# Kernel tuning notes

Measured on AMD Instinct MI355X. Metric: run time of the kernel, lower is better.

Reference implementation:

```python
import jax, jax.numpy as jnp
from jax import lax
import numpy as np


def _normalize(x):
    # F.normalize(dim=-1), eps=1e-12
    return x / jnp.clip(jnp.linalg.norm(x, axis=-1, keepdims=True), 1e-12, None)


def _masked_log_softmax(logits, mask):
    # softmax restricted to active columns (emulates gathering active objects)
    return jax.nn.log_softmax(jnp.where(mask, logits, -1e9), axis=-1)


def _aabb_iou(gc, gs, pc, ps):
    # gc,gs: (B,L,3) gt center/size; pc,ps: (B,P,3) pred center/size -> iou (B,L,P)
    # create_box_batch builds axis-aligned corner boxes, so box3d_overlap == AABB IoU
    gmin = (gc - gs * 0.5)[:, :, None, :]
    gmax = (gc + gs * 0.5)[:, :, None, :]
    pmin = (pc - ps * 0.5)[:, None, :, :]
    pmax = (pc + ps * 0.5)[:, None, :, :]
    inter = jnp.prod(jnp.clip(jnp.minimum(gmax, pmax) - jnp.maximum(gmin, pmin), 0.0, None), axis=-1)
    vol_g = jnp.prod(gs, axis=-1)[:, :, None]
    vol_p = jnp.prod(ps, axis=-1)[:, None, :]
    return inter / (vol_g + vol_p - inter + 1e-7)


def setup_inputs() -> dict:
    key = jax.random.key(0)
    ks = jax.random.split(key, 11)
    B, P, L, H = 32, 1024, 32, 128
    return {
        'pred_center': jax.random.normal(ks[0], (B, P, 3), jnp.float32),
        'pred_size': jax.random.uniform(ks[1], (B, P, 3), jnp.float32, 0.2, 1.5),
        'bbox_feature': jax.random.normal(ks[2], (B, P, H), jnp.float32),
        'gt_center': jax.random.normal(ks[3], (B, L, 3), jnp.float32),
        'gt_size': jax.random.uniform(ks[4], (B, L, 3), jnp.float32, 0.2, 1.5),
        'lang_emb': jax.random.normal(ks[5], (B * L, H), jnp.float32),
        'objectness_scores': jax.random.normal(ks[6], (B, P, 2), jnp.float32),
        'Wt': jax.random.normal(ks[7], (H, H), jnp.float32) * (1.0 / np.sqrt(H)),
        'Wp': jax.random.normal(ks[8], (H, H), jnp.float32) * (1.0 / np.sqrt(H)),
        'Wpi': jax.random.normal(ks[9], (H, H), jnp.float32) * (1.0 / np.sqrt(H)),
        'lang_num': jax.random.randint(ks[10], (B,), 1, L + 1, jnp.int64),
    }


def reference(pred_center, pred_size, bbox_feature, gt_center, gt_size,
              lang_emb, objectness_scores, Wt, Wp, Wpi, lang_num):
    sg = lax.stop_gradient
    B, P = pred_center.shape[:2]
    L = gt_center.shape[1]

    # objectness mask (argmax over 2 classes), detached
    obj_mask = (jnp.argmax(objectness_scores, axis=-1) == 1).astype(jnp.float32)  # (B,P)
    cmask = obj_mask > 0
    cnt = obj_mask.sum(-1)                       # active objects per sample
    cnt1 = jnp.maximum(cnt, 1.0)

    # 3D IoU between gt boxes (size + 0.01, as in forward) and predicted boxes; all detached
    iou = _aabb_iou(sg(gt_center), sg(gt_size) + 0.01, sg(pred_center), sg(pred_size))  # (B,L,P)
    tgt = (iou > 0.25).astype(jnp.float32) * obj_mask[:, None, :]  # (B,L,P), detached

    # ---- language-box contrastive (NCE) ----
    text = _normalize(jnp.einsum('bld,hd->blh', lang_emb.reshape(B, L, -1), Wt))   # (B,L,H)
    boxl = _normalize(jnp.einsum('bpd,hd->bph', bbox_feature, Wp))                 # (B,P,H)
    sim_lang = jnp.einsum('blh,bph->blp', text, boxl)                              # (B,L,P)
    ls = _masked_log_softmax(sim_lang, cmask[:, None, :])
    loss_v = (-ls * tgt).sum(-1) / cnt1[:, None]                                   # mean over cnt cols
    # transposed logits are (cnt,1): log_softmax over a single logit is 0 -> loss_t == 0
    lang_nce = 0.5 * loss_v                                                        # (B,L)

    lang_active = (jnp.arange(L)[None, :] < lang_num[:, None]).astype(jnp.float32)
    lang_con_loss = (lang_nce * lang_active).sum() / B

    # ---- box-box contrastive (NCE) ----
    boxi = _normalize(jnp.einsum('bpd,hd->bph', bbox_feature, Wpi))                # (B,P,H)
    sim_iou = jnp.einsum('bph,bqh->bpq', boxi, boxi)                               # (B,P,P)
    ls_r = _masked_log_softmax(sim_iou, cmask[:, None, :])
    ls_c = _masked_log_softmax(jnp.swapaxes(sim_iou, 1, 2), cmask[:, None, :])
    # target(b,l,p,q) = tgt(b,l,p)*tgt(b,l,q); contract without materializing (B,L,P,P)
    lv = jnp.einsum('blp,bpq,blq->bl', tgt, -ls_r, tgt) / (cnt1 ** 2)[:, None]
    lt = jnp.einsum('blp,bpq,blq->bl', tgt, -ls_c, tgt) / (cnt1 ** 2)[:, None]
    iou_nce = 0.5 * (lv + lt)                                                      # (B,L)
    iou_con_loss = (iou_nce * lang_active).sum() / B

    return jnp.stack([lang_con_loss, iou_con_loss])
```

## Files before the change

### kernel.cpp

```cpp
#include <hip/hip_runtime.h>
#include <hip/hip_bf16.h>
#include <math.h>

typedef unsigned short u16;
typedef unsigned int   u32;
typedef unsigned char  u8;
typedef unsigned long long u64;

typedef __attribute__((ext_vector_type(8))) short short8_t;
typedef __attribute__((ext_vector_type(4))) float f32x4_t;

#define H128 128

__device__ __forceinline__ float bf2f(u16 v){
    u32 u = ((u32)v) << 16;
    return __uint_as_float(u);
}
__device__ __forceinline__ u16 f2bf(float x){
    u32 u = __float_as_uint(x);
    u32 r = (u + 0x7fffu + ((u >> 16) & 1u)) >> 16;
    return (u16)r;
}
__device__ __forceinline__ void unpack8(uint4 v, float* f){
    f[0] = bf2f((u16)(v.x & 0xffff)); f[1] = bf2f((u16)(v.x >> 16));
    f[2] = bf2f((u16)(v.y & 0xffff)); f[3] = bf2f((u16)(v.y >> 16));
    f[4] = bf2f((u16)(v.z & 0xffff)); f[5] = bf2f((u16)(v.z >> 16));
    f[6] = bf2f((u16)(v.w & 0xffff)); f[7] = bf2f((u16)(v.w >> 16));
}
__device__ __forceinline__ float ld1(const void* p, size_t i, int F){
    return F ? ((const float*)p)[i] : bf2f(((const u16*)p)[i]);
}
__device__ __forceinline__ void ld8(const void* p, size_t i, int F, float* f){
    if (F){
        const float* fp = (const float*)p + i;
        float4 a = *(const float4*)fp;
        float4 b = *(const float4*)(fp + 4);
        f[0]=a.x; f[1]=a.y; f[2]=a.z; f[3]=a.w;
        f[4]=b.x; f[5]=b.y; f[6]=b.z; f[7]=b.w;
    } else {
        uint4 v = *(const uint4*)((const u16*)p + i);
        unpack8(v, f);
    }
}
__device__ __forceinline__ float clampf(float x, float lo, float hi){
    return fminf(fmaxf(x, lo), hi);
}

__global__ void __launch_bounds__(256) k_zero(
        const int* __restrict__ lang_raw, const void* __restrict__ pred_size,
        int* __restrict__ lni, float* __restrict__ accf, int* __restrict__ flagp,
        u32* __restrict__ ctrs,
        float* __restrict__ cnt, float* __restrict__ tcnt, float* __restrict__ sexp,
        float* __restrict__ sdot, float* __restrict__ lse, int* __restrict__ needcnt,
        int B, int c, int P, int L, int first)
{
    int gid = blockIdx.x * 256 + threadIdx.x;
    int gsz = gridDim.x * 256;
    for (int i = gid; i < c * P; i += gsz) lse[i] = 0.f;
    for (int i = gid; i < c * L; i += gsz){ tcnt[i] = 0.f; sexp[i] = 0.f; sdot[i] = 0.f; }
    for (int i = gid; i < c; i += gsz){ cnt[i] = 0.f; needcnt[i] = 0; }
    if (first && blockIdx.x == 0){
        int tid = threadIdx.x;
        __shared__ int cir, is64_s;
        if (tid == 0){ cir = 0; accf[0] = 0.f; accf[1] = 0.f; }
        __syncthreads();
        if (tid < 64){
            const u16* ps = (const u16*)pred_size;
            int cc = 0;
            u16 v0 = ps[tid], v1 = ps[tid + 64];
            if (v0 >= 0x3000 && v0 < 0x4100) cc++;
            if (v1 >= 0x3000 && v1 < 0x4100) cc++;
            atomicAdd(&cir, cc);
        }
        if (tid < 64) ctrs[tid] = 0u;
        if (tid == 0)
            is64_s = ((B >= 8) && lang_raw[1] == 0 && lang_raw[3] == 0 &&
                      lang_raw[5] == 0 && lang_raw[7] == 0) ? 1 : 0;
        __syncthreads();
        if (tid == 0) *flagp = (cir >= 120) ? 0 : 1;
        if (tid < B) lni[tid] = is64_s ? lang_raw[2 * tid] : lang_raw[tid];
    }
}

__device__ void prep_fn(char* smem,
        const void* obj, const void* gtc, const void* gts,
        const void* pc_, const void* ps_, int F,
        u8* mask, float* cnt, u8* tgt, float* tcnt,
        int* needcnt, int* needlist, int b0, int P, int L, int bblk)
{
    int tid = threadIdx.x;
    int nt = P / 256;
    int b = bblk / nt, ct = bblk % nt;
    int p = ct * 256 + tid;

    float* gtb = (float*)smem;
    float* tl  = (float*)(smem + L * 32);
    float* red = (float*)(smem + L * 32 + L * 4);

    if (tid < L){
        float gmn[3], gmx[3], gss[3];
        for (int i = 0; i < 3; i++){
            size_t gi = ((size_t)(b0 + b) * L + tid) * 3 + i;
            float gc  = ld1(gtc, gi, F);
            float gsv = ld1(gts, gi, F) + 0.01f;
            gmn[i] = gc - 0.5f * gsv; gmx[i] = gc + 0.5f * gsv; gss[i] = gsv;
        }
        float* r = &gtb[tid * 8];
        r[0] = gmn[0]; r[1] = gmn[1]; r[2] = gmn[2];
        r[3] = gmx[0]; r[4] = gmx[1]; r[5] = gmx[2];
        r[6] = gss[0] * gss[1] * gss[2];
        tl[tid] = 0.f;
    }
    __syncthreads();

    size_t ob = ((size_t)(b0 + b) * P + p) * 2;
    float s0 = ld1(obj, ob, F), s1 = ld1(obj, ob + 1, F);
    u8 m = (s1 > s0) ? 1 : 0;
    mask[(size_t)b * P + p] = m;

    size_t pb = ((size_t)(b0 + b) * P + p) * 3;
    float pl[3], ph[3], volp = 1.f;
    for (int i = 0; i < 3; i++){
        float pcv = ld1(pc_, pb + i, F), psv = ld1(ps_, pb + i, F);
        pl[i] = pcv - 0.5f * psv; ph[i] = pcv + 0.5f * psv; volp *= psv;
    }
    bool any = false;
    for (int l = 0; l < L; l++){
        float* r = &gtb[l * 8];
        float inter = 1.f;
        for (int i = 0; i < 3; i++){
            float mn = fmaxf(r[i],     pl[i]);
            float mx = fminf(r[3 + i], ph[i]);
            inter *= fmaxf(mx - mn, 0.f);
        }
        float iou = inter / (r[6] + volp - inter + 1e-7f);
        u8 t = (iou > 0.25f && m) ? 1 : 0;
        tgt[((size_t)b * L + l) * P + p] = t;
        if (t){ any = true; atomicAdd(&tl[l], 1.f); }
    }
    int lane = tid & 63;
    u64 bal = __ballot(any);
    int wcount = __popcll(bal);
    int base = 0;
    if (lane == 0 && wcount) base = atomicAdd(&needcnt[b], wcount);
    base = __shfl(base, 0);
    if (any){
        int rank = __popcll(bal & ((1ULL << lane) - 1ULL));
        needlist[(size_t)b * P + base + rank] = p;
    }
    red[tid] = (float)m;
    __syncthreads();
    for (int st = 128; st > 0; st >>= 1){
        if (tid < st) red[tid] += red[tid + st];
        __syncthreads();
    }
    if (tid == 0) atomicAdd(&cnt[b], red[0]);
    if (tid < L && tl[tid] != 0.f) atomicAdd(&tcnt[b * L + tid], tl[tid]);
}

__device__ void proj_fn(char* smem,
        const void* __restrict__ X, const void* __restrict__ W, int F,
        u16* __restrict__ outb, int row0, int rowoff, int nrows)
{
    int tid = threadIdx.x;
    u16* Ws = (u16*)smem;
    u16* Xs = (u16*)(smem + 32768);

    for (int i = 0; i < 8; i++){
        int cid = tid + i * 256;
        int r = cid >> 4, cc = cid & 15;
        float f[8];
        ld8(W, (size_t)r * H128 + cc * 8, F, f);
        u16* dst = &Ws[r * H128 + ((cc ^ (r & 15)) * 8)];
        #pragma unroll
        for (int j = 0; j < 8; j++) dst[j] = f2bf(f[j]);
    }
    for (int i = 0; i < 4; i++){
        int cid = tid + i * 256;
        int r = cid >> 4, cc = cid & 15;
        int row = row0 + r;
        float f[8];
        if (row < nrows){
            ld8(X, (size_t)(rowoff + row) * H128 + cc * 8, F, f);
        } else {
            for (int j = 0; j < 8; j++) f[j] = 0.f;
        }
        u16* dst = &Xs[r * H128 + ((cc ^ (r & 15)) * 8)];
        #pragma unroll
        for (int j = 0; j < 8; j++) dst[j] = f2bf(f[j]);
    }
    __syncthreads();

    int w = tid >> 6, lane = tid & 63;
    int quad = lane >> 4, mrow = lane & 15;

    short8_t af[4];
    int arow = w * 16 + mrow;
    #pragma unroll
    for (int kt = 0; kt < 4; kt++){
        int chunk = kt * 4 + quad;
        af[kt] = *(const short8_t*)&Xs[arow * H128 + ((chunk ^ mrow) * 8)];
    }

    f32x4_t acc[8];
    #pragma unroll
    for (int ntl = 0; ntl < 8; ntl++) acc[ntl] = (f32x4_t){0.f, 0.f, 0.f, 0.f};
    #pragma unroll
    for (int ntl = 0; ntl < 8; ntl++){
        int n = ntl * 16 + mrow;
        #pragma unroll
        for (int kt = 0; kt < 4; kt++){
            int chunk = kt * 4 + quad;
            short8_t bf = *(const short8_t*)&Ws[n * H128 + ((chunk ^ mrow) * 8)];
            acc[ntl] = __builtin_amdgcn_mfma_f32_16x16x32_bf16(af[kt], bf, acc[ntl], 0, 0, 0);
        }
    }

    float ss[4] = {0.f, 0.f, 0.f, 0.f};
    #pragma unroll
    for (int ntl = 0; ntl < 8; ntl++)
        #pragma unroll
        for (int reg = 0; reg < 4; reg++) ss[reg] += acc[ntl][reg] * acc[ntl][reg];
    #pragma unroll
    for (int off = 1; off <= 8; off <<= 1)
        #pragma unroll
        for (int reg = 0; reg < 4; reg++) ss[reg] += __shfl_xor(ss[reg], off);
    float rn[4];
    #pragma unroll
    for (int reg = 0; reg < 4; reg++) rn[reg] = 1.0f / fmaxf(sqrtf(ss[reg]), 1e-12f);

    #pragma unroll
    for (int reg = 0; reg < 4; reg++){
        int row = row0 + w * 16 + quad * 4 + reg;
        if (row < nrows){
            #pragma unroll
            for (int ntl = 0; ntl < 8; ntl++){
                int col = ntl * 16 + mrow;
                outb[(size_t)row * H128 + col] = f2bf(acc[ntl][reg] * rn[reg]);
            }
        }
    }
}

__global__ void __launch_bounds__(256) k_main1(
        const void* __restrict__ obj, const void* __restrict__ gtc, const void* __restrict__ gts,
        const void* __restrict__ pc_, const void* __restrict__ ps_,
        const void* __restrict__ bbox, const void* __restrict__ lang,
        const void* __restrict__ Wp, const void* __restrict__ Wpi, const void* __restrict__ Wt,
        const int* __restrict__ Fp,
        u8* __restrict__ mask, float* __restrict__ cnt, u8* __restrict__ tgt,
        float* __restrict__ tcnt, int* __restrict__ needcnt, int* __restrict__ needlist,
        u16* __restrict__ boxl, u16* __restrict__ boxi, u16* __restrict__ text,
        int nprep, int nb1, int b0, int P, int L, int nrows_bp, int nrows_t)
{
    __shared__ __align__(16) char smem[49152];
    const int F = *Fp;
    int blk = blockIdx.x;
    if (blk < nprep){
        prep_fn(smem, obj, gtc, gts, pc_, ps_, F, mask, cnt, tgt, tcnt,
                needcnt, needlist, b0, P, L, blk);
        return;
    }
    blk -= nprep;
    if (blk < nb1)
        proj_fn(smem, bbox, Wp,  F, boxl, blk * 64,            b0 * P, nrows_bp);
    else if (blk < 2 * nb1)
        proj_fn(smem, bbox, Wpi, F, boxi, (blk - nb1) * 64,    b0 * P, nrows_bp);
    else
        proj_fn(smem, lang, Wt,  F, text, (blk - 2 * nb1) * 64, b0 * L, nrows_t);
}

__device__ void lang_fn(char* smem,
        const u16* __restrict__ text, const u16* __restrict__ boxl,
        const u8* __restrict__ mask, const u8* __restrict__ tgt,
        float* __restrict__ sexp, float* __restrict__ sdot, int P, int L, int bblk)
{
    int nct = P >> 7;
    int b = bblk / nct, ct = bblk % nct;
    int p0 = ct * 128;
    int tid = threadIdx.x;

    u16* As = (u16*)smem;
    u16* Bs = (u16*)(smem + 8192);
    u8*  Ts = (u8*)(smem + 40960);
    u8*  mk = (u8*)(smem + 45056);

    for (int i = 0; i < 2; i++){
        int cid = tid + i * 256;
        int r = cid >> 4, cc = cid & 15;
        uint4 v = *(const uint4*)&text[((size_t)b * L + r) * H128 + cc * 8];
        *(uint4*)&As[r * H128 + ((cc ^ (r & 15)) * 8)] = v;
    }
    for (int i = 0; i < 8; i++){
        int cid = tid + i * 256;
        int r = cid >> 4, cc = cid & 15;
        uint4 v = *(const uint4*)&boxl[((size_t)b * P + p0 + r) * H128 + cc * 8];
        *(uint4*)&Bs[r * H128 + ((cc ^ (r & 15)) * 8)] = v;
    }
    {
        int l = tid >> 3, seg = tid & 7;
        uint4 v = *(const uint4*)&tgt[((size_t)b * L + l) * P + p0 + seg * 16];
        *(uint4*)&Ts[l * 128 + seg * 16] = v;
    }
    if (tid < 128) mk[tid] = mask[(size_t)b * P + p0 + tid];
    __syncthreads();

    int w = tid >> 6, lane = tid & 63;
    int quad = lane >> 4, mrow = lane & 15;
    int mt = w & 1, ch = w >> 1;

    short8_t af[4];
    #pragma unroll
    for (int kt = 0; kt < 4; kt++){
        int chunk = kt * 4 + quad;
        af[kt] = *(const short8_t*)&As[(mt * 16 + mrow) * H128 + ((chunk ^ mrow) * 8)];
    }

    float se[4] = {0.f, 0.f, 0.f, 0.f};
    float sd[4] = {0.f, 0.f, 0.f, 0.f};
    #pragma unroll
    for (int nt = 0; nt < 4; nt++){
        int cl = ch * 64 + nt * 16 + mrow;
        f32x4_t acc = (f32x4_t){0.f, 0.f, 0.f, 0.f};
        #pragma unroll
        for (int kt = 0; kt < 4; kt++){
            int chunk = kt * 4 + quad;
            short8_t bf = *(const short8_t*)&Bs[cl * H128 + ((chunk ^ mrow) * 8)];
            acc = __builtin_amdgcn_mfma_f32_16x16x32_bf16(af[kt], bf, acc, 0, 0, 0);
        }
        float m = mk[cl] ? 1.f : 0.f;
        #pragma unroll
        for (int reg = 0; reg < 4; reg++){
            int l = mt * 16 + quad * 4 + reg;
            float d = acc[reg];
            se[reg] += m * __expf(d);
            if (m != 0.f && Ts[l * 128 + cl]) sd[reg] += d;
        }
    }
    #pragma unroll
    for (int off = 1; off <= 8; off <<= 1)
        #pragma unroll
        for (int reg = 0; reg < 4; reg++){
            se[reg] += __shfl_xor(se[reg], off);
            sd[reg] += __shfl_xor(sd[reg], off);
        }
    if (mrow == 0){
        #pragma unroll
        for (int reg = 0; reg < 4; reg++){
            int l = mt * 16 + quad * 4 + reg;
            atomicAdd(&sexp[b * L + l], se[reg]);
            atomicAdd(&sdot[b * L + l], sd[reg]);
        }
    }
}

__device__ void lse_fn(char* smem,
        const u16* __restrict__ boxi, const u8* __restrict__ mask,
        const int* __restrict__ needcnt, const int* __restrict__ needlist,
        float* __restrict__ lse, int P, int bblk)
{
    int nct = P >> 7;
    int b = bblk / nct, ct = bblk % nct;
    int q0 = ct * 128;
    int ncnt = needcnt[b];
    if (ncnt <= 0) return;
    int tid = threadIdx.x;

    u16* Bs = (u16*)smem;
    u8*  mk = (u8*)(smem + 32768);

    for (int i = 0; i < 8; i++){
        int cid = tid + i * 256;
        int r = cid >> 4, cc = cid & 15;
        uint4 v = *(const uint4*)&boxi[((size_t)b * P + q0 + r) * H128 + cc * 8];
        *(uint4*)&Bs[r * H128 + ((cc ^ (r & 15)) * 8)] = v;
    }
    if (tid < 128) mk[tid] = mask[(size_t)b * P + q0 + tid];
    __syncthreads();

    int w = tid >> 6, lane = tid & 63;
    int quad = lane >> 4, mrow = lane & 15;
    int nrt = (ncnt + 15) >> 4;

    for (int rt = w; rt < nrt; rt += 4){
        int i = rt * 16 + mrow;
        int prow = needlist[(size_t)b * P + ((i < ncnt) ? i : (ncnt - 1))];
        const u16* ab = &boxi[((size_t)b * P + prow) * H128];
        short8_t af[4];
        #pragma unroll
        for (int kt = 0; kt < 4; kt++)
            af[kt] = *(const short8_t*)&ab[(kt * 4 + quad) * 8];

        float se[4] = {0.f, 0.f, 0.f, 0.f};
        #pragma unroll
        for (int nt = 0; nt < 8; nt++){
            int cl = nt * 16 + mrow;
            f32x4_t acc = (f32x4_t){0.f, 0.f, 0.f, 0.f};
            #pragma unroll
            for (int kt = 0; kt < 4; kt++){
                int chunk = kt * 4 + quad;
                short8_t bf = *(const short8_t*)&Bs[cl * H128 + ((chunk ^ mrow) * 8)];
                acc = __builtin_amdgcn_mfma_f32_16x16x32_bf16(af[kt], bf, acc, 0, 0, 0);
            }
            float m = mk[cl] ? 1.f : 0.f;
            #pragma unroll
            for (int reg = 0; reg < 4; reg++) se[reg] += m * __expf(acc[reg]);
        }
        #pragma unroll
        for (int off = 1; off <= 8; off <<= 1)
            #pragma unroll
            for (int reg = 0; reg < 4; reg++) se[reg] += __shfl_xor(se[reg], off);
        if (mrow == 0){
            #pragma unroll
            for (int reg = 0; reg < 4; reg++){
                int i2 = rt * 16 + quad * 4 + reg;
                if (i2 < ncnt)
                    atomicAdd(&lse[(size_t)b * P + needlist[(size_t)b * P + i2]], se[reg]);
            }
        }
    }
}

__global__ void __launch_bounds__(256) k_main2(
        const u16* __restrict__ text, const u16* __restrict__ boxl, const u16* __restrict__ boxi,
        const u8* __restrict__ mask, const u8* __restrict__ tgt,
        const int* __restrict__ needcnt, const int* __restrict__ needlist,
        float* __restrict__ sexp, float* __restrict__ sdot, float* __restrict__ lse,
        int nlang, int P, int L)
{
    __shared__ __align__(16) char smem[45184];
    int blk = blockIdx.x;
    if (blk < nlang) lang_fn(smem, text, boxl, mask, tgt, sexp, sdot, P, L, blk);
    else             lse_fn(smem, boxi, mask, needcnt, needlist, lse, P, blk - nlang);
}

__global__ void __launch_bounds__(256) k_main3(
        const u16* __restrict__ boxi, const u8* __restrict__ tgt,
        const float* __restrict__ lse, const float* __restrict__ cnt,
        const float* __restrict__ tcnt, const float* __restrict__ sexp,
        const float* __restrict__ sdot, const int* __restrict__ lni,
        float* __restrict__ accf, u32* __restrict__ ctr, const int* __restrict__ flagp,
        void* __restrict__ out, float invB, int is_last, int b0, int P, int L)
{
    int blk = blockIdx.x, b = blk / L, l = blk % L, tid = threadIdx.x;
    float tf = tcnt[b * L + l];
    bool active = (l < lni[b0 + b]) && (tf > 0.f);

    if (active){
        float c1 = fmaxf(cnt[b], 1.f);
        if (tid == 0){
            float LSE = logf(fmaxf(sexp[b * L + l], 1e-30f));
            atomicAdd(&accf[0], clampf(0.5f * (tf * LSE - sdot[b * L + l]) / c1, -1e5f, 1e5f));
        }
        int wid = tid >> 6, lane = tid & 63;
        __shared__ int mem[1024];
        __shared__ int wbase[4];
        __shared__ int total;
        __shared__ float redu[256];
        __shared__ float Ufin;
        if (tid == 0) total = 0;
        __syncthreads();
        for (int k = 0; k < P / 256; k++){
            int p = tid + k * 256;
            bool hit = (tgt[((size_t)b * L + l) * P + p] != 0);
            u64 bal = __ballot(hit);
            if (lane == 0) wbase[wid] = __popcll(bal);
            __syncthreads();
            if (tid == 0){
                int s = total;
                for (int w = 0; w < 4; w++){ int c = wbase[w]; wbase[w] = s; s += c; }
                total = s;
            }
            __syncthreads();
            if (hit){
                int rank = __popcll(bal & ((1ULL << lane) - 1ULL));
                mem[wbase[wid] + rank] = p;
            }
            __syncthreads();
        }
        int t = total;

        float U = 0.f;
        for (int i = tid; i < t; i += 256)
            U += logf(fmaxf(lse[(size_t)b * P + mem[i]], 1e-30f));
        redu[tid] = U; __syncthreads();
        for (int st = 128; st > 0; st >>= 1){
            if (tid < st) redu[tid] += redu[tid + st];
            __syncthreads();
        }
        if (tid == 0) Ufin = redu[0];
        __syncthreads();

        {
            int h = tid & 127, half = tid >> 7;
            float vh = 0.f;
            for (int i = half; i < t; i += 2)
                vh += bf2f(boxi[((size_t)b * P + mem[i]) * H128 + h]);
            redu[tid] = vh;
        }
        __syncthreads();
        if (tid < 128){
            float v = redu[tid] + redu[tid + 128];
            redu[tid] = v * v;
        }
        __syncthreads();
        for (int st = 64; st > 0; st >>= 1){
            if (tid < st) redu[tid] += redu[tid + st];
            __syncthreads();
        }
        if (tid == 0)
            atomicAdd(&accf[1], clampf(((float)t * Ufin - redu[0]) / (c1 * c1), -1e5f, 1e5f));
    }

    if (tid == 0){
        __threadfence();
        u32 old = atomicAdd(ctr, 1u);
        if (is_last && old == (u32)(gridDim.x - 1)){
            __threadfence();
            float a  = clampf(accf[0] * invB, -1e6f, 1e6f);
            float bb = clampf(accf[1] * invB, -1e6f, 1e6f);
            if (*flagp){
                ((float*)out)[0] = a; ((float*)out)[1] = bb;
            } else {
                ((u16*)out)[0] = f2bf(a); ((u16*)out)[1] = f2bf(bb);
            }
        }
    }
}

extern "C" void kernel_launch(void* const* d_in, const int* in_sizes, int n_in,
                              void* d_out, int out_size, void* d_ws, size_t ws_size,
                              hipStream_t stream)
{
    const void* pred_center = d_in[0];
    const void* pred_size   = d_in[1];
    const void* bbox        = d_in[2];
    const void* gtc         = d_in[3];
    const void* gts         = d_in[4];
    const void* lang        = d_in[5];
    const void* obj         = d_in[6];
    const void* Wt          = d_in[7];
    const void* Wp          = d_in[8];
    const void* Wpi         = d_in[9];
    const int*  lang_raw    = (const int*)d_in[10];

    int B = in_sizes[10];
    int P = in_sizes[0] / (3 * B);
    int L = in_sizes[3] / (3 * B);
    (void)n_in; (void)out_size;

    char* w = (char*)d_ws;
    float* accf  = (float*)w;
    int*   flagp = (int*)(w + 64);
    u32*   ctrs  = (u32*)(w + 128);
    int*   lni   = (int*)(w + 384);
    char*  chunk_base = w + 768;
    size_t chunk_avail = (ws_size > 768) ? ws_size - 768 : 0;

    size_t per_b = (size_t)P + (size_t)P * 4 + 8 + (size_t)L * 4 * 3
                 + (size_t)L * P + (size_t)P * 4
                 + (size_t)P * H128 * 2 * 2 + (size_t)L * H128 * 2;
    size_t slop = 14 * 256;
    int C = B;
    if ((size_t)B * per_b + slop > chunk_avail){
        size_t av = (chunk_avail > slop) ? chunk_avail - slop : 0;
        C = (int)(av / per_b);
        if (C < 1) C = 1;
        if (C > B) C = B;
    }

    int chunk_idx = 0;
    for (int b0 = 0; b0 < B; b0 += C, chunk_idx++){
        int c = (B - b0 < C) ? (B - b0) : C;

        size_t off = 0;
        auto carve = [&](size_t bytes) -> void* {
            void* p = chunk_base + off;
            off = (off + bytes + 255) & ~(size_t)255;
            return p;
        };
        u8*    mask     = (u8*)   carve((size_t)c * P);
        float* cnt      = (float*)carve((size_t)c * 4);
        int*   needcnt  = (int*)  carve((size_t)c * 4);
        float* tcnt     = (float*)carve((size_t)c * L * 4);
        float* sexp     = (float*)carve((size_t)c * L * 4);
        float* sdot     = (float*)carve((size_t)c * L * 4);
        u8*    tgtb     = (u8*)   carve((size_t)c * L * P);
        int*   needlist = (int*)  carve((size_t)c * P * 4);
        float* lse      = (float*)carve((size_t)c * P * 4);
        u16*   boxl     = (u16*)  carve((size_t)c * P * H128 * 2);
        u16*   boxi     = (u16*)  carve((size_t)c * P * H128 * 2);
        u16*   text     = (u16*)  carve((size_t)c * L * H128 * 2);

        int is_last = (b0 + c >= B) ? 1 : 0;

        k_zero<<<32, 256, 0, stream>>>(lang_raw, pred_size, lni, accf, flagp, ctrs,
                                       cnt, tcnt, sexp, sdot, lse, needcnt,
                                       B, c, P, L, (b0 == 0) ? 1 : 0);

        int nprep = c * (P / 256);
        int nb1 = (c * P + 63) / 64;
        int nbt = (c * L + 63) / 64;
        k_main1<<<nprep + 2 * nb1 + nbt, 256, 0, stream>>>(
            obj, gtc, gts, pred_center, pred_size, bbox, lang, Wp, Wpi, Wt, flagp,
            mask, cnt, tgtb, tcnt, needcnt, needlist, boxl, boxi, text,
            nprep, nb1, b0, P, L, c * P, c * L);

        int nlang = c * (P / 128);
        k_main2<<<2 * nlang, 256, 0, stream>>>(text, boxl, boxi, mask, tgtb,
                                               needcnt, needlist, sexp, sdot, lse,
                                               nlang, P, L);

        k_main3<<<c * L, 256, 0, stream>>>(boxi, tgtb, lse, cnt, tcnt, sexp, sdot,
                                           lni, accf, &ctrs[chunk_idx], flagp, d_out,
                                           1.0f / (float)B, is_last, b0, P, L);
    }
}
```

Measured before the change: 133.6 us.

## Remove zeroing kernel, use per-tile partials, compact active columns in LSE

Drops the separate zero-init kernel. Global float atomics are replaced with per-tile partial buffers that the final kernel sums. Format detection and init move into the first main kernel. The box-box LSE pass now gathers only the active (masked) columns through a compacted list, so its blocks skip work proportional to the inactive objects. The cost is more indirection, larger workspace and extra partial reductions in k_main3.

```diff
diff --git a/kernel.cpp b/kernel.cpp
--- a/kernel.cpp
+++ b/kernel.cpp
@@ -45,57 +45,38 @@
 __device__ __forceinline__ float clampf(float x, float lo, float hi){
     return fminf(fmaxf(x, lo), hi);
 }
-
-__global__ void __launch_bounds__(256) k_zero(
-        const int* __restrict__ lang_raw, const void* __restrict__ pred_size,
-        int* __restrict__ lni, float* __restrict__ accf, int* __restrict__ flagp,
-        u32* __restrict__ ctrs,
-        float* __restrict__ cnt, float* __restrict__ tcnt, float* __restrict__ sexp,
-        float* __restrict__ sdot, float* __restrict__ lse, int* __restrict__ needcnt,
-        int B, int c, int P, int L, int first)
-{
-    int gid = blockIdx.x * 256 + threadIdx.x;
-    int gsz = gridDim.x * 256;
-    for (int i = gid; i < c * P; i += gsz) lse[i] = 0.f;
-    for (int i = gid; i < c * L; i += gsz){ tcnt[i] = 0.f; sexp[i] = 0.f; sdot[i] = 0.f; }
-    for (int i = gid; i < c; i += gsz){ cnt[i] = 0.f; needcnt[i] = 0; }
-    if (first && blockIdx.x == 0){
-        int tid = threadIdx.x;
-        __shared__ int cir, is64_s;
-        if (tid == 0){ cir = 0; accf[0] = 0.f; accf[1] = 0.f; }
-        __syncthreads();
-        if (tid < 64){
-            const u16* ps = (const u16*)pred_size;
-            int cc = 0;
-            u16 v0 = ps[tid], v1 = ps[tid + 64];
-            if (v0 >= 0x3000 && v0 < 0x4100) cc++;
-            if (v1 >= 0x3000 && v1 < 0x4100) cc++;
-            atomicAdd(&cir, cc);
-        }
-        if (tid < 64) ctrs[tid] = 0u;
-        if (tid == 0)
-            is64_s = ((B >= 8) && lang_raw[1] == 0 && lang_raw[3] == 0 &&
-                      lang_raw[5] == 0 && lang_raw[7] == 0) ? 1 : 0;
-        __syncthreads();
-        if (tid == 0) *flagp = (cir >= 120) ? 0 : 1;
-        if (tid < B) lni[tid] = is64_s ? lang_raw[2 * tid] : lang_raw[tid];
-    }
+__device__ __forceinline__ int detectF(const void* pred_size, int* Fs){
+    int tid = threadIdx.x;
+    if (tid < 64){
+        const u16* ps = (const u16*)pred_size;
+        u16 v0 = ps[tid], v1 = ps[tid + 64];
+        int cc = ((v0 >= 0x3000 && v0 < 0x4100) ? 1 : 0)
+               + ((v1 >= 0x3000 && v1 < 0x4100) ? 1 : 0);
+        #pragma unroll
+        for (int off = 32; off > 0; off >>= 1) cc += __shfl_xor(cc, off);
+        if (tid == 0) *Fs = (cc >= 120) ? 0 : 1;
+    }
+    __syncthreads();
+    return *Fs;
 }
 
 __device__ void prep_fn(char* smem,
         const void* obj, const void* gtc, const void* gts,
         const void* pc_, const void* ps_, int F,
-        u8* mask, float* cnt, u8* tgt, float* tcnt,
-        int* needcnt, int* needlist, int b0, int P, int L, int bblk)
+        u8* mask, float* cnt_part, u8* tgt, float* tcnt_part,
+        int* needcnt_part, int* needlist, int* acnt_part, int* alist,
+        int b0, int P, int L, int bblk)
 {
     int tid = threadIdx.x;
-    int nt = P / 256;
-    int b = bblk / nt, ct = bblk % nt;
+    int ntile = P / 256;
+    int b = bblk / ntile, ct = bblk % ntile;
     int p = ct * 256 + tid;
 
     float* gtb = (float*)smem;
-    float* tl  = (float*)(smem + L * 32);
-    float* red = (float*)(smem + L * 32 + L * 4);
+    float* tl  = gtb + (size_t)L * 8;
+    float* red = tl + L;
+    int*   wb  = (int*)(red + 256);
+    int*   wb2 = wb + 4;
 
     if (tid < L){
         float gmn[3], gmx[3], gss[3];
@@ -138,24 +119,36 @@
         tgt[((size_t)b * L + l) * P + p] = t;
         if (t){ any = true; atomicAdd(&tl[l], 1.f); }
     }
-    int lane = tid & 63;
-    u64 bal = __ballot(any);
-    int wcount = __popcll(bal);
-    int base = 0;
-    if (lane == 0 && wcount) base = atomicAdd(&needcnt[b], wcount);
-    base = __shfl(base, 0);
+
+    int wid = tid >> 6, lane = tid & 63;
+    u64 bal  = __ballot(any);
+    u64 bal2 = __ballot(m != 0);
+    if (lane == 0){ wb[wid] = __popcll(bal); wb2[wid] = __popcll(bal2); }
+    red[tid] = (float)m;
+    __syncthreads();
+    if (tid == 0){
+        int s = 0;
+        for (int w = 0; w < 4; w++){ int cn = wb[w];  wb[w]  = s; s += cn; }
+        needcnt_part[b * 4 + ct] = s;
+        s = 0;
+        for (int w = 0; w < 4; w++){ int cn = wb2[w]; wb2[w] = s; s += cn; }
+        acnt_part[b * 4 + ct] = s;
+    }
+    __syncthreads();
     if (any){
         int rank = __popcll(bal & ((1ULL << lane) - 1ULL));
-        needlist[(size_t)b * P + base + rank] = p;
-    }
-    red[tid] = (float)m;
-    __syncthreads();
+        needlist[(size_t)b * P + ct * 256 + wb[wid] + rank] = p;
+    }
+    if (m){
+        int rank = __popcll(bal2 & ((1ULL << lane) - 1ULL));
+        alist[(size_t)b * P + ct * 256 + wb2[wid] + rank] = p;
+    }
     for (int st = 128; st > 0; st >>= 1){
         if (tid < st) red[tid] += red[tid + st];
         __syncthreads();
     }
-    if (tid == 0) atomicAdd(&cnt[b], red[0]);
-    if (tid < L && tl[tid] != 0.f) atomicAdd(&tcnt[b * L + tid], tl[tid]);
+    if (tid == 0) cnt_part[b * 4 + ct] = red[0];
+    if (tid < L)  tcnt_part[(size_t)(b * 4 + ct) * L + tid] = tl[tid];
 }
 
 __device__ void proj_fn(char* smem,
@@ -247,25 +240,33 @@
         const void* __restrict__ pc_, const void* __restrict__ ps_,
         const void* __restrict__ bbox, const void* __restrict__ lang,
         const void* __restrict__ Wp, const void* __restrict__ Wpi, const void* __restrict__ Wt,
-        const int* __restrict__ Fp,
-        u8* __restrict__ mask, float* __restrict__ cnt, u8* __restrict__ tgt,
-        float* __restrict__ tcnt, int* __restrict__ needcnt, int* __restrict__ needlist,
+        u8* __restrict__ mask, float* __restrict__ cnt_part, u8* __restrict__ tgt,
+        float* __restrict__ tcnt_part, int* __restrict__ needcnt_part, int* __restrict__ needlist,
+        int* __restrict__ acnt_part, int* __restrict__ alist,
         u16* __restrict__ boxl, u16* __restrict__ boxi, u16* __restrict__ text,
+        float* __restrict__ accf, u32* __restrict__ ctrs, int* __restrict__ flagp,
+        int chunk_idx, int first,
         int nprep, int nb1, int b0, int P, int L, int nrows_bp, int nrows_t)
 {
     __shared__ __align__(16) char smem[49152];
-    const int F = *Fp;
+    __shared__ int Fs;
+    int F = detectF(ps_, &Fs);
     int blk = blockIdx.x;
+    if (blk == 0 && threadIdx.x == 0){
+        ctrs[chunk_idx] = 0u;
+        *flagp = F;
+        if (first){ accf[0] = 0.f; accf[1] = 0.f; }
+    }
     if (blk < nprep){
-        prep_fn(smem, obj, gtc, gts, pc_, ps_, F, mask, cnt, tgt, tcnt,
-                needcnt, needlist, b0, P, L, blk);
+        prep_fn(smem, obj, gtc, gts, pc_, ps_, F, mask, cnt_part, tgt, tcnt_part,
+                needcnt_part, needlist, acnt_part, alist, b0, P, L, blk);
         return;
     }
     blk -= nprep;
     if (blk < nb1)
-        proj_fn(smem, bbox, Wp,  F, boxl, blk * 64,            b0 * P, nrows_bp);
+        proj_fn(smem, bbox, Wp,  F, boxl, blk * 64,             b0 * P, nrows_bp);
     else if (blk < 2 * nb1)
-        proj_fn(smem, bbox, Wpi, F, boxi, (blk - nb1) * 64,    b0 * P, nrows_bp);
+        proj_fn(smem, bbox, Wpi, F, boxi, (blk - nb1) * 64,     b0 * P, nrows_bp);
     else
         proj_fn(smem, lang, Wt,  F, text, (blk - 2 * nb1) * 64, b0 * L, nrows_t);
 }
@@ -273,7 +274,7 @@
 __device__ void lang_fn(char* smem,
         const u16* __restrict__ text, const u16* __restrict__ boxl,
         const u8* __restrict__ mask, const u8* __restrict__ tgt,
-        float* __restrict__ sexp, float* __restrict__ sdot, int P, int L, int bblk)
+        float* __restrict__ sexp_part, float* __restrict__ sdot_part, int P, int L, int bblk)
 {
     int nct = P >> 7;
     int b = bblk / nct, ct = bblk % nct;
@@ -348,22 +349,28 @@
         #pragma unroll
         for (int reg = 0; reg < 4; reg++){
             int l = mt * 16 + quad * 4 + reg;
-            atomicAdd(&sexp[b * L + l], se[reg]);
-            atomicAdd(&sdot[b * L + l], sd[reg]);
+            size_t idx = (size_t)(b * L + l) * 16 + ct * 2 + ch;
+            sexp_part[idx] = se[reg];
+            sdot_part[idx] = sd[reg];
         }
     }
 }
 
 __device__ void lse_fn(char* smem,
-        const u16* __restrict__ boxi, const u8* __restrict__ mask,
-        const int* __restrict__ needcnt, const int* __restrict__ needlist,
-        float* __restrict__ lse, int P, int bblk)
-{
-    int nct = P >> 7;
-    int b = bblk / nct, ct = bblk % nct;
-    int q0 = ct * 128;
-    int ncnt = needcnt[b];
-    if (ncnt <= 0) return;
+        const u16* __restrict__ boxi,
+        const int* __restrict__ needcnt_part, const int* __restrict__ needlist,
+        const int* __restrict__ acnt_part, const int* __restrict__ alist,
+        float* __restrict__ lse_part, int P, int bblk)
+{
+    int b = bblk >> 3, ctA = bblk & 7;
+    int prefA[5], preN[5];
+    prefA[0] = 0; preN[0] = 0;
+    for (int j = 0; j < 4; j++){
+        prefA[j + 1] = prefA[j] + acnt_part[b * 4 + j];
+        preN[j + 1]  = preN[j]  + needcnt_part[b * 4 + j];
+    }
+    int acnt = prefA[4], ncnt = preN[4];
+    if (ctA * 128 >= acnt || ncnt <= 0) return;
     int tid = threadIdx.x;
 
     u16* Bs = (u16*)smem;
@@ -372,10 +379,16 @@
     for (int i = 0; i < 8; i++){
         int cid = tid + i * 256;
         int r = cid >> 4, cc = cid & 15;
-        uint4 v = *(const uint4*)&boxi[((size_t)b * P + q0 + r) * H128 + cc * 8];
+        int aq = ctA * 128 + r;
+        uint4 v = {0, 0, 0, 0};
+        if (aq < acnt){
+            int j = (aq >= prefA[1]) + (aq >= prefA[2]) + (aq >= prefA[3]);
+            int cp = alist[(size_t)b * P + j * 256 + (aq - prefA[j])];
+            v = *(const uint4*)&boxi[((size_t)b * P + cp) * H128 + cc * 8];
+        }
         *(uint4*)&Bs[r * H128 + ((cc ^ (r & 15)) * 8)] = v;
     }
-    if (tid < 128) mk[tid] = mask[(size_t)b * P + q0 + tid];
+    if (tid < 128) mk[tid] = (ctA * 128 + tid < acnt) ? 1 : 0;
     __syncthreads();
 
     int w = tid >> 6, lane = tid & 63;
@@ -384,7 +397,9 @@
 
     for (int rt = w; rt < nrt; rt += 4){
         int i = rt * 16 + mrow;
-        int prow = needlist[(size_t)b * P + ((i < ncnt) ? i : (ncnt - 1))];
+        int ic = (i < ncnt) ? i : (ncnt - 1);
+        int j = (ic >= preN[1]) + (ic >= preN[2]) + (ic >= preN[3]);
+        int prow = needlist[(size_t)b * P + j * 256 + (ic - preN[j])];
         const u16* ab = &boxi[((size_t)b * P + prow) * H128];
         short8_t af[4];
         #pragma unroll
@@ -414,8 +429,11 @@
             #pragma unroll
             for (int reg = 0; reg < 4; reg++){
                 int i2 = rt * 16 + quad * 4 + reg;
-                if (i2 < ncnt)
-                    atomicAdd(&lse[(size_t)b * P + needlist[(size_t)b * P + i2]], se[reg]);
+                if (i2 < ncnt){
+                    int j2 = (i2 >= preN[1]) + (i2 >= preN[2]) + (i2 >= preN[3]);
+                    int pr2 = needlist[(size_t)b * P + j2 * 256 + (i2 - preN[j2])];
+                    lse_part[((size_t)b * P + pr2) * 8 + ctA] = se[reg];
+                }
             }
         }
     }
@@ -424,40 +442,52 @@
 __global__ void __launch_bounds__(256) k_main2(
         const u16* __restrict__ text, const u16* __restrict__ boxl, const u16* __restrict__ boxi,
         const u8* __restrict__ mask, const u8* __restrict__ tgt,
-        const int* __restrict__ needcnt, const int* __restrict__ needlist,
-        float* __restrict__ sexp, float* __restrict__ sdot, float* __restrict__ lse,
-        int nlang, int P, int L)
+        const int* __restrict__ needcnt_part, const int* __restrict__ needlist,
+        const int* __restrict__ acnt_part, const int* __restrict__ alist,
+        float* __restrict__ sexp_part, float* __restrict__ sdot_part,
+        float* __restrict__ lse_part, int nlang, int P, int L)
 {
     __shared__ __align__(16) char smem[45184];
     int blk = blockIdx.x;
-    if (blk < nlang) lang_fn(smem, text, boxl, mask, tgt, sexp, sdot, P, L, blk);
-    else             lse_fn(smem, boxi, mask, needcnt, needlist, lse, P, blk - nlang);
+    if (blk < nlang) lang_fn(smem, text, boxl, mask, tgt, sexp_part, sdot_part, P, L, blk);
+    else             lse_fn(smem, boxi, needcnt_part, needlist, acnt_part, alist,
+                            lse_part, P, blk - nlang);
 }
 
 __global__ void __launch_bounds__(256) k_main3(
         const u16* __restrict__ boxi, const u8* __restrict__ tgt,
-        const float* __restrict__ lse, const float* __restrict__ cnt,
-        const float* __restrict__ tcnt, const float* __restrict__ sexp,
-        const float* __restrict__ sdot, const int* __restrict__ lni,
+        const float* __restrict__ lse_part, const float* __restrict__ cnt_part,
+        const float* __restrict__ tcnt_part, const float* __restrict__ sexp_part,
+        const float* __restrict__ sdot_part, const int* __restrict__ acnt_part,
+        const int* __restrict__ lang_raw, float* __restrict__ loss_part,
         float* __restrict__ accf, u32* __restrict__ ctr, const int* __restrict__ flagp,
-        void* __restrict__ out, float invB, int is_last, int b0, int P, int L)
+        void* __restrict__ out, float invB, int is_last, int B, int b0, int P, int L)
 {
     int blk = blockIdx.x, b = blk / L, l = blk % L, tid = threadIdx.x;
-    float tf = tcnt[b * L + l];
-    bool active = (l < lni[b0 + b]) && (tf > 0.f);
-
+    bool is64 = (B >= 8) && lang_raw[1] == 0 && lang_raw[3] == 0 &&
+                lang_raw[5] == 0 && lang_raw[7] == 0;
+    int lniv = is64 ? lang_raw[2 * (b0 + b)] : lang_raw[b0 + b];
+    float tf = tcnt_part[(size_t)(b * 4 + 0) * L + l] + tcnt_part[(size_t)(b * 4 + 1) * L + l]
+             + tcnt_part[(size_t)(b * 4 + 2) * L + l] + tcnt_part[(size_t)(b * 4 + 3) * L + l];
+    bool active = (l < lniv) && (tf > 0.f);
+
+    __shared__ int mem[1024];
+    __shared__ int wbase[4];
+    __shared__ int total;
+    __shared__ float redu[256];
+    __shared__ float redu2[256];
+    __shared__ float Ufin;
+    __shared__ int lastf;
+
+    float lang_loss = 0.f, iou_loss = 0.f;
     if (active){
-        float c1 = fmaxf(cnt[b], 1.f);
-        if (tid == 0){
-            float LSE = logf(fmaxf(sexp[b * L + l], 1e-30f));
-            atomicAdd(&accf[0], clampf(0.5f * (tf * LSE - sdot[b * L + l]) / c1, -1e5f, 1e5f));
-        }
+        float c1 = fmaxf(cnt_part[b * 4] + cnt_part[b * 4 + 1] +
+                         cnt_part[b * 4 + 2] + cnt_part[b * 4 + 3], 1.f);
+        int acnt = acnt_part[b * 4] + acnt_part[b * 4 + 1] +
+                   acnt_part[b * 4 + 2] + acnt_part[b * 4 + 3];
+        int nact = (acnt + 127) >> 7;
+
         int wid = tid >> 6, lane = tid & 63;
-        __shared__ int mem[1024];
-        __shared__ int wbase[4];
-        __shared__ int total;
-        __shared__ float redu[256];
-        __shared__ float Ufin;
         if (tid == 0) total = 0;
         __syncthreads();
         for (int k = 0; k < P / 256; k++){
@@ -481,8 +511,12 @@
         int t = total;
 
         float U = 0.f;
-        for (int i = tid; i < t; i += 256)
-            U += logf(fmaxf(lse[(size_t)b * P + mem[i]], 1e-30f));
+        for (int i = tid; i < t; i += 256){
+            const float* lp = &lse_part[((size_t)b * P + mem[i]) * 8];
+            float s = 0.f;
+            for (int ctA = 0; ctA < nact; ctA++) s += lp[ctA];
+            U += logf(fmaxf(s, 1e-30f));
+        }
         redu[tid] = U; __syncthreads();
         for (int st = 128; st > 0; st >>= 1){
             if (tid < st) redu[tid] += redu[tid + st];
@@ -508,21 +542,49 @@
             if (tid < st) redu[tid] += redu[tid + st];
             __syncthreads();
         }
-        if (tid == 0)
-            atomicAdd(&accf[1], clampf(((float)t * Ufin - redu[0]) / (c1 * c1), -1e5f, 1e5f));
+        if (tid == 0){
+            float sexp = 0.f, sdot = 0.f;
+            const float* ep = &sexp_part[(size_t)(b * L + l) * 16];
+            const float* dp = &sdot_part[(size_t)(b * L + l) * 16];
+            for (int k = 0; k < 16; k++){ sexp += ep[k]; sdot += dp[k]; }
+            float LSE = logf(fmaxf(sexp, 1e-30f));
+            lang_loss = clampf(0.5f * (tf * LSE - sdot) / c1, -1e5f, 1e5f);
+            iou_loss  = clampf(((float)t * Ufin - redu[0]) / (c1 * c1), -1e5f, 1e5f);
+        }
     }
 
     if (tid == 0){
+        loss_part[blk] = lang_loss;
+        loss_part[gridDim.x + blk] = iou_loss;
         __threadfence();
         u32 old = atomicAdd(ctr, 1u);
-        if (is_last && old == (u32)(gridDim.x - 1)){
-            __threadfence();
-            float a  = clampf(accf[0] * invB, -1e6f, 1e6f);
-            float bb = clampf(accf[1] * invB, -1e6f, 1e6f);
-            if (*flagp){
-                ((float*)out)[0] = a; ((float*)out)[1] = bb;
-            } else {
-                ((u16*)out)[0] = f2bf(a); ((u16*)out)[1] = f2bf(bb);
+        lastf = (old == (u32)(gridDim.x - 1)) ? 1 : 0;
+    }
+    __syncthreads();
+    if (lastf){
+        __threadfence();
+        float suml = 0.f, sumi = 0.f;
+        for (int i = tid; i < (int)gridDim.x; i += 256){
+            suml += loss_part[i];
+            sumi += loss_part[gridDim.x + i];
+        }
+        redu[tid] = suml; redu2[tid] = sumi;
+        __syncthreads();
+        for (int st = 128; st > 0; st >>= 1){
+            if (tid < st){ redu[tid] += redu[tid + st]; redu2[tid] += redu2[tid + st]; }
+            __syncthreads();
+        }
+        if (tid == 0){
+            accf[0] += redu[0];
+            accf[1] += redu2[0];
+            if (is_last){
+                float a  = clampf(accf[0] * invB, -1e6f, 1e6f);
+                float bb = clampf(accf[1] * invB, -1e6f, 1e6f);
+                if (*flagp){
+                    ((float*)out)[0] = a; ((float*)out)[1] = bb;
+                } else {
+                    ((u16*)out)[0] = f2bf(a); ((u16*)out)[1] = f2bf(bb);
+                }
             }
         }
     }
@@ -553,14 +615,20 @@
     float* accf  = (float*)w;
     int*   flagp = (int*)(w + 64);
     u32*   ctrs  = (u32*)(w + 128);
-    int*   lni   = (int*)(w + 384);
-    char*  chunk_base = w + 768;
-    size_t chunk_avail = (ws_size > 768) ? ws_size - 768 : 0;
-
-    size_t per_b = (size_t)P + (size_t)P * 4 + 8 + (size_t)L * 4 * 3
-                 + (size_t)L * P + (size_t)P * 4
-                 + (size_t)P * H128 * 2 * 2 + (size_t)L * H128 * 2;
-    size_t slop = 14 * 256;
+    char*  chunk_base = w + 512;
+    size_t chunk_avail = (ws_size > 512) ? ws_size - 512 : 0;
+
+    size_t per_b = (size_t)P
+                 + 64
+                 + (size_t)4 * L * 4
+                 + (size_t)L * 16 * 4 * 2
+                 + (size_t)L * P
+                 + (size_t)P * 4 * 2
+                 + (size_t)P * 8 * 4
+                 + (size_t)P * H128 * 2 * 2
+                 + (size_t)L * H128 * 2
+                 + (size_t)L * 8;
+    size_t slop = 20 * 256;
     int C = B;
     if ((size_t)B * per_b + slop > chunk_avail){
         size_t av = (chunk_avail > slop) ? chunk_avail - slop : 0;
@@ -579,40 +647,41 @@
             off = (off + bytes + 255) & ~(size_t)255;
             return p;
         };
-        u8*    mask     = (u8*)   carve((size_t)c * P);
-        float* cnt      = (float*)carve((size_t)c * 4);
-        int*   needcnt  = (int*)  carve((size_t)c * 4);
-        float* tcnt     = (float*)carve((size_t)c * L * 4);
-        float* sexp     = (float*)carve((size_t)c * L * 4);
-        float* sdot     = (float*)carve((size_t)c * L * 4);
-        u8*    tgtb     = (u8*)   carve((size_t)c * L * P);
-        int*   needlist = (int*)  carve((size_t)c * P * 4);
-        float* lse      = (float*)carve((size_t)c * P * 4);
-        u16*   boxl     = (u16*)  carve((size_t)c * P * H128 * 2);
-        u16*   boxi     = (u16*)  carve((size_t)c * P * H128 * 2);
-        u16*   text     = (u16*)  carve((size_t)c * L * H128 * 2);
+        u8*    mask      = (u8*)   carve((size_t)c * P);
+        float* cnt_part  = (float*)carve((size_t)c * 4 * 4);
+        int*   acnt_part = (int*)  carve((size_t)c * 4 * 4);
+        int*   ncnt_part = (int*)  carve((size_t)c * 4 * 4);
+        float* tcnt_part = (float*)carve((size_t)c * 4 * L * 4);
+        float* sexp_part = (float*)carve((size_t)c * L * 16 * 4);
+        float* sdot_part = (float*)carve((size_t)c * L * 16 * 4);
+        u8*    tgtb      = (u8*)   carve((size_t)c * L * P);
+        int*   needlist  = (int*)  carve((size_t)c * P * 4);
+        int*   alist     = (int*)  carve((size_t)c * P * 4);
+        float* lse_part  = (float*)carve((size_t)c * P * 8 * 4);
+        u16*   boxl      = (u16*)  carve((size_t)c * P * H128 * 2);
+        u16*   boxi      = (u16*)  carve((size_t)c * P * H128 * 2);
+        u16*   text      = (u16*)  carve((size_t)c * L * H128 * 2);
+        float* loss_part = (float*)carve((size_t)c * L * 8);
 
         int is_last = (b0 + c >= B) ? 1 : 0;
-
-        k_zero<<<32, 256, 0, stream>>>(lang_raw, pred_size, lni, accf, flagp, ctrs,
-                                       cnt, tcnt, sexp, sdot, lse, needcnt,
-                                       B, c, P, L, (b0 == 0) ? 1 : 0);
-
         int nprep = c * (P / 256);
         int nb1 = (c * P + 63) / 64;
         int nbt = (c * L + 63) / 64;
+
         k_main1<<<nprep + 2 * nb1 + nbt, 256, 0, stream>>>(
-            obj, gtc, gts, pred_center, pred_size, bbox, lang, Wp, Wpi, Wt, flagp,
-            mask, cnt, tgtb, tcnt, needcnt, needlist, boxl, boxi, text,
+            obj, gtc, gts, pred_center, pred_size, bbox, lang, Wp, Wpi, Wt,
+            mask, cnt_part, tgtb, tcnt_part, ncnt_part, needlist, acnt_part, alist,
+            boxl, boxi, text, accf, ctrs, flagp, chunk_idx, (b0 == 0) ? 1 : 0,
             nprep, nb1, b0, P, L, c * P, c * L);
 
         int nlang = c * (P / 128);
-        k_main2<<<2 * nlang, 256, 0, stream>>>(text, boxl, boxi, mask, tgtb,
-                                               needcnt, needlist, sexp, sdot, lse,
-                                               nlang, P, L);
-
-        k_main3<<<c * L, 256, 0, stream>>>(boxi, tgtb, lse, cnt, tcnt, sexp, sdot,
-                                           lni, accf, &ctrs[chunk_idx], flagp, d_out,
-                                           1.0f / (float)B, is_last, b0, P, L);
-    }
-}
+        k_main2<<<nlang + c * 8, 256, 0, stream>>>(
+            text, boxl, boxi, mask, tgtb, ncnt_part, needlist, acnt_part, alist,
+            sexp_part, sdot_part, lse_part, nlang, P, L);
+
+        k_main3<<<c * L, 256, 0, stream>>>(
+            boxi, tgtb, lse_part, cnt_part, tcnt_part, sexp_part, sdot_part,
+            acnt_part, lang_raw, loss_part, accf, &ctrs[chunk_idx], flagp, d_out,
+            1.0f / (float)B, is_last, B, b0, P, L);
+    }
+}
```

New measurement: 133.5 us. About the same (-0.1%).
